# Kernel tuning notes

Measured on AMD Instinct MI355X. Metric: run time of the kernel, lower is better.

The kernel has to match this reference:

```python
import jax, jax.numpy as jnp
from jax import lax
import numpy as np

B = 8; T = 64000
NFFT = 1024; HOP = 256
SC = 20; KS = 1024; PAD = 512
HEADS = 8; GH = 64; GO = 32
SPEC_DIM = 32 * (NFFT // 4) // 2   # 4096
NODE_DIM = SC + SPEC_DIM           # 4116
EPS = 1e-5
NEG_SLOPE = 0.2


def setup_inputs() -> dict:
    ks = jax.random.split(jax.random.key(0), 12)
    f32 = jnp.float32
    def rn(k, shp, s):
        return jax.random.normal(k, shp, dtype=f32) * s
    return {
        "x": jax.random.normal(ks[0], (B, 1, T), dtype=f32),
        "sinc_w": rn(ks[1], (SC, 1, KS), 0.03),
        "conv1_w": rn(ks[2], (32, 1, 3, 3), 0.1),
        "conv1_b": jnp.zeros((32,), f32),
        "bn1_g": jnp.ones((32,), f32),
        "bn1_b": jnp.zeros((32,), f32),
        "conv2_w": rn(ks[3], (32, 32, 3, 3), 0.06),
        "conv2_b": jnp.zeros((32,), f32),
        "bn2_g": jnp.ones((32,), f32),
        "bn2_b": jnp.zeros((32,), f32),
        "gat1_W": rn(ks[4], (NODE_DIM, HEADS * GH), 0.015),
        "gat1_asrc": rn(ks[5], (HEADS, GH), 0.1),
        "gat1_adst": rn(ks[6], (HEADS, GH), 0.1),
        "gat1_bias": jnp.zeros((HEADS * GH,), f32),
        "gat2_W": rn(ks[7], (HEADS * GH, GO), 0.04),
        "gat2_asrc": rn(ks[8], (1, GO), 0.1),
        "gat2_adst": rn(ks[9], (1, GO), 0.1),
        "gat2_bias": jnp.zeros((GO,), f32),
        "fc1_w": rn(ks[10], (GO, 128), 0.15),
        "fc1_b": jnp.zeros((128,), f32),
        "bnf_g": jnp.ones((128,), f32),
        "bnf_b": jnp.zeros((128,), f32),
        "fc2_w": rn(ks[11], (128, 2), 0.08),
        "fc2_b": jnp.zeros((2,), f32),
    }


def _bn2d_eval(z, g, b):
    # eval-mode BatchNorm2d with running_mean=0, running_var=1
    s = g / jnp.sqrt(1.0 + EPS)
    return z * s[None, :, None, None] + b[None, :, None, None]


def _conv2d(z, w, b):
    y = lax.conv_general_dilated(z, w, (1, 1), ((1, 1), (1, 1)),
                                 dimension_numbers=("NCHW", "OIHW", "NCHW"))
    return y + b[None, :, None, None]


def _gat_dense(hin, W, asrc, adst, bias, heads, fo, concat):
    # PyG GATConv on a fully-connected graph (add_self_loops=True default
    # => every node attends to all nodes including itself). Eval mode (no dropout).
    b, n, d = hin.shape
    h = jnp.einsum("bnd,dhf->bnhf", hin, W.reshape(d, heads, fo))
    s_src = jnp.einsum("bnhf,hf->bnh", h, asrc)   # alpha_j contribution
    s_dst = jnp.einsum("bnhf,hf->bnh", h, adst)   # alpha_i contribution
    e = jax.nn.leaky_relu(s_dst[:, :, None, :] + s_src[:, None, :, :], NEG_SLOPE)  # (b,i,j,h)
    a = jax.nn.softmax(e, axis=2)                 # softmax over sources j per dest i
    out = jnp.einsum("bijh,bjhf->bihf", a, h)
    out = out.reshape(b, n, heads * fo) if concat else out.mean(axis=2)
    return out + bias


def reference(x, sinc_w, conv1_w, conv1_b, bn1_g, bn1_b, conv2_w, conv2_b,
              bn2_g, bn2_b, gat1_W, gat1_asrc, gat1_adst, gat1_bias,
              gat2_W, gat2_asrc, gat2_adst, gat2_bias,
              fc1_w, fc1_b, bnf_g, bnf_b, fc2_w, fc2_b):
    b = x.shape[0]
    # --- sinc (band-pass) conv branch: conv1d k=1024, pad=512 ---
    sinc = lax.conv_general_dilated(x, sinc_w, (1,), ((PAD, PAD),),
                                    dimension_numbers=("NCH", "OIH", "NCH"))  # (b,20,T+1)
    Ls = (sinc.shape[-1] // 4) * 4
    sinc_feat = sinc[:, :, :Ls].reshape(b, SC, Ls // 4, 4).mean(-1)  # avg_pool1d(4)
    sinc_feat = jnp.transpose(sinc_feat, (0, 2, 1))                  # (b, Ls//4, 20)

    # --- STFT branch (torch.stft: center=True, reflect pad, rect window) ---
    xw = x[:, 0, :]
    xp = jnp.pad(xw, ((0, 0), (NFFT // 2, NFFT // 2)), mode="reflect")
    n_frames = 1 + T // HOP  # 251
    idx = np.arange(n_frames)[:, None] * HOP + np.arange(NFFT)
    frames = xp[:, idx]                                   # (b, 251, 1024)
    mag = jnp.abs(jnp.fft.rfft(frames, axis=-1))          # (b, 251, 513)
    logmag = jnp.log(mag + 1e-9)
    s = jnp.transpose(logmag, (0, 2, 1))[:, None]         # (b, 1, 513, 251)

    h = jax.nn.relu(_bn2d_eval(_conv2d(s, conv1_w, conv1_b), bn1_g, bn1_b))
    h = jax.nn.relu(_bn2d_eval(_conv2d(h, conv2_w, conv2_b), bn2_g, bn2_b))
    Fq = (h.shape[2] // 2) * 2
    Tt = (h.shape[3] // 2) * 2
    h = h[:, :, :Fq, :Tt].reshape(b, 32, Fq // 2, 2, Tt // 2, 2).max(axis=(3, 5))  # maxpool 2x2
    spec_feat = jnp.transpose(h, (0, 3, 1, 2)).reshape(b, -1, SPEC_DIM)  # (b, 250, 4096)

    n = min(sinc_feat.shape[1], spec_feat.shape[1])  # 250
    nodes = jnp.concatenate([sinc_feat[:, :n], spec_feat[:, :n]], axis=-1)  # (b,250,4116)

    g1 = jax.nn.relu(_gat_dense(nodes, gat1_W, gat1_asrc, gat1_adst, gat1_bias, HEADS, GH, True))
    g2 = _gat_dense(g1, gat2_W, gat2_asrc, gat2_adst, gat2_bias, 1, GO, False)
    emb = g2.mean(axis=1)  # (b, 32) graph-mean readout

    z = emb @ fc1_w + fc1_b
    z = jax.nn.relu(z * (bnf_g / jnp.sqrt(1.0 + EPS)) + bnf_b)  # eval BN1d
    out = z @ fc2_w + fc2_b
    return (out, emb)
```

## Files before the change

kernel.cpp:

```cpp
#include <hip/hip_runtime.h>
#include <hip/hip_bf16.h>
#include <math.h>

#define TB 8
#define TT 64000
#define NFRAMES 251
#define NROWS (TB*NFRAMES)
#define GROWS 2048
#define NBINS 513
#define NBPAD 576
#define NNODE 250
#define NODE_DIM 4116
#define KPAD 4128

typedef __attribute__((ext_vector_type(8))) short short8;
typedef __attribute__((ext_vector_type(4))) float floatx4;

static __device__ __forceinline__ unsigned short f2bf(float x) {
    __hip_bfloat16 h = __float2bfloat16(x);
    return *(unsigned short*)&h;
}
static __device__ __forceinline__ float bf2f(unsigned short u) {
    __hip_bfloat16 h = *(__hip_bfloat16*)&u;
    return __bfloat162float(h);
}

__global__ __launch_bounds__(256) void k_prep(
    const float* __restrict__ x, const float* __restrict__ sinc_w,
    const float* __restrict__ c2w, const float* __restrict__ g2bn,
    const float* __restrict__ c1w, const float* __restrict__ g1bn,
    const float* __restrict__ W,
    unsigned short* __restrict__ fh, unsigned short* __restrict__ fl,
    unsigned short* __restrict__ bch, unsigned short* __restrict__ bcl,
    unsigned short* __restrict__ bsh, unsigned short* __restrict__ bsl,
    unsigned short* __restrict__ wbt, unsigned short* __restrict__ Bp,
    unsigned short* __restrict__ Bc1,
    unsigned short* __restrict__ Wt, unsigned short* __restrict__ nodesb,
    unsigned short* __restrict__ h1t, unsigned short* __restrict__ h2t) {
    __shared__ unsigned short tile[64][65];
    int bi = blockIdx.x, tid = threadIdx.x;
    if (bi < 2048) {
        int idx = bi * 256 + tid;
        int row = idx >> 8, r = idx & 255;
        int b = row >> 8, j = row & 255;
        int u = j * 256 + r - 512;
        if (u < 0) u = -u;
        if (u >= TT) u = 2 * TT - 2 - u;
        float v = x[b * TT + u];
        unsigned short h = f2bf(v);
        fh[idx] = h;
        fl[idx] = f2bf(v - bf2f(h));
    } else if (bi < 2624) {
        int idx = (bi - 2048) * 256 + tid;
        int k = idx >> 8, r = idx & 255;
        float s = 0.f, c = 0.f;
        if (k < NBINS) {
            int mm = (k * r) & 1023;
            sincospif((float)mm * (1.0f / 512.0f), &s, &c);
        }
        unsigned short chv = f2bf(c), shv = f2bf(s);
        bch[idx] = chv; bcl[idx] = f2bf(c - bf2f(chv));
        bsh[idx] = shv; bsl[idx] = f2bf(s - bf2f(shv));
    } else if (bi < 3144) {
        int local = bi - 2624;
        int kt = local % 65, nt = local / 65;
        for (int idx = tid; idx < 4096; idx += 256) {
            int r = idx >> 6, c = idx & 63;
            int kp = kt * 64 + r;
            int k;
            if (kp < 20) k = kp;
            else if (kp < NODE_DIM) { int t = kp - 20; k = 20 + (t & 15) * 256 + (t >> 4); }
            else k = -1;
            float v = (k >= 0) ? W[k * 512 + nt * 64 + c] : 0.f;
            tile[r][c] = f2bf(v);
        }
        __syncthreads();
        for (int idx = tid; idx < 4096; idx += 256) {
            int nl = idx >> 6, kl = idx & 63;
            int k = kt * 64 + kl;
            if (k < KPAD)
                Wt[(size_t)(nt * 64 + nl) * KPAD + k] = tile[kl][nl];
        }
    } else if (bi < 3276) {
        int idx = (bi - 3144) * 256 + tid;
        if (idx < 32 * 1056) {
            int c = idx / 1056, m = idx - c * 1056;
            float s = 0.f;
            if (c < 20 && m < 1027) {
                #pragma unroll
                for (int d = 0; d < 4; d++) {
                    int k = m - d;
                    if (k >= 0 && k < 1024) s += sinc_w[c * 1024 + k];
                }
                s *= 0.25f;
            }
            wbt[idx] = f2bf(s);
        }
    } else if (bi < 3312) {
        int idx = (bi - 3276) * 256 + tid;
        if (idx < 9216) {
            int j = idx & 7, lane = (idx >> 3) & 63, ct = (idx >> 9) & 1, s = idx >> 10;
            int co = ct * 16 + (lane & 15);
            int ci = (lane >> 4) * 8 + j;
            float inv = rsqrtf(1.0f + 1e-5f);
            Bp[idx] = f2bf(c2w[co * 288 + ci * 9 + s] * (g2bn[co] * inv));
        }
    } else if (bi < 3508) {
        int idx = (bi - 3312) * 256 + tid;
        if (idx < 24000) {
            int row = idx / 12, c = idx - row * 12;
            nodesb[(size_t)row * KPAD + 4116 + c] = 0;
        } else if (idx < 48576) {
            int t = idx - 24000; int r = t / 6, c = t - r * 6;
            h1t[(size_t)r * 256 + 250 + c] = 0;
        } else if (idx < 50112) {
            int t = idx - 48576; int r = t / 6, c = t - r * 6;
            h2t[(size_t)r * 256 + 250 + c] = 0;
        }
    } else {
        int idx = (bi - 3508) * 256 + tid;
        if (idx < 1024) {
            int ch = idx >> 5, k = idx & 31;
            float inv = rsqrtf(1.0f + 1e-5f);
            int t; int typ;
            if (k < 8)       { t = k;      typ = 0; }
            else if (k < 16) { t = k - 8;  typ = 0; }
            else if (k < 24) { t = k - 16; typ = 1; }
            else if (k == 24 || k == 25) { t = 8; typ = 0; }
            else if (k == 26) { t = 8; typ = 1; }
            else { t = 0; typ = 2; }
            unsigned short outv = 0;
            if (typ != 2) {
                float wv = c1w[ch * 9 + t] * (g1bn[ch] * inv);
                unsigned short whi = f2bf(wv);
                outv = (typ == 0) ? whi : f2bf(wv - bf2f(whi));
            }
            Bc1[idx] = outv;
        }
    }
}

__global__ __launch_bounds__(256) void k_sincm(const float* __restrict__ x,
                                               const unsigned short* __restrict__ wbt,
                                               unsigned short* __restrict__ nodesb) {
    __shared__ __align__(16) unsigned short xs[1312];
    int ut = blockIdx.x, b = blockIdx.y;
    int tid = threadIdx.x;
    int base = 256 * ut - 512;
    for (int i = tid; i < 1312; i += 256) {
        int g = base + i;
        float v = (g >= 0 && g < TT) ? x[b * TT + g] : 0.f;
        xs[i] = f2bf(v);
    }
    __syncthreads();
    int w = tid >> 6, lane = tid & 63;
    int q = lane >> 4, col = lane & 15;
    floatx4 acc[2];
    acc[0] = acc[1] = (floatx4){0.f, 0.f, 0.f, 0.f};
    for (int K0 = 0; K0 < 1056; K0 += 32) {
        int off = 4 * (w * 16 + col) + K0 + q * 8;
        unsigned long long lo = *(const unsigned long long*)&xs[off];
        unsigned long long hi = *(const unsigned long long*)&xs[off + 4];
        union { unsigned long long u64[2]; short8 s8; } cv;
        cv.u64[0] = lo; cv.u64[1] = hi;
        short8 af = cv.s8;
        #pragma unroll
        for (int ni = 0; ni < 2; ni++) {
            short8 bf = *(const short8*)(wbt + (size_t)(ni * 16 + col) * 1056 + K0 + q * 8);
            acc[ni] = __builtin_amdgcn_mfma_f32_16x16x32_bf16(af, bf, acc[ni], 0, 0, 0);
        }
    }
    #pragma unroll
    for (int ni = 0; ni < 2; ni++)
        #pragma unroll
        for (int rr = 0; rr < 4; rr++) {
            int u = ut * 64 + w * 16 + q * 4 + rr;
            int c = ni * 16 + col;
            if (u < NNODE && c < 20)
                nodesb[(size_t)(b * NNODE + u) * KPAD + c] = f2bf(acc[ni][rr]);
        }
}

__global__ __launch_bounds__(256) void k_dft_mfma(const unsigned short* __restrict__ fh,
                                                  const unsigned short* __restrict__ fl,
                                                  const unsigned short* __restrict__ ch,
                                                  const unsigned short* __restrict__ cl,
                                                  const unsigned short* __restrict__ sh,
                                                  const unsigned short* __restrict__ sl,
                                                  float* __restrict__ GRo,
                                                  float* __restrict__ GIo) {
    __shared__ __align__(16) unsigned short Ah[32 * 40];
    __shared__ __align__(16) unsigned short Al[32 * 40];
    __shared__ __align__(16) unsigned short Bch[64 * 40];
    __shared__ __align__(16) unsigned short Bcl[64 * 40];
    __shared__ __align__(16) unsigned short Bsh[64 * 40];
    __shared__ __align__(16) unsigned short Bsl[64 * 40];
    int tid = threadIdx.x;
    int N0 = blockIdx.x * 64, M0 = blockIdx.y * 32;
    int br = tid >> 2, bc = (tid & 3) * 8;
    size_t boff = (size_t)(N0 + br) * 256 + bc;
    int ar = (tid & 127) >> 2, ac = (tid & 3) * 8;
    size_t aoff = (size_t)(M0 + ar) * 256 + ac;
    bool loA = tid < 128;
    int w = tid >> 6, lane = tid & 63;
    int q = lane >> 4, col = lane & 15;
    int mb = (w >> 1) * 16, nb = (w & 1) * 32;
    floatx4 aR[2], aI[2];
    aR[0] = aR[1] = aI[0] = aI[1] = (floatx4){0.f, 0.f, 0.f, 0.f};

    for (int K0 = 0; K0 < 256; K0 += 32) {
        if (loA) *(short8*)&Ah[ar * 40 + ac] = *(const short8*)(fh + aoff + K0);
        else     *(short8*)&Al[ar * 40 + ac] = *(const short8*)(fl + aoff + K0);
        *(short8*)&Bch[br * 40 + bc] = *(const short8*)(ch + boff + K0);
        *(short8*)&Bcl[br * 40 + bc] = *(const short8*)(cl + boff + K0);
        *(short8*)&Bsh[br * 40 + bc] = *(const short8*)(sh + boff + K0);
        *(short8*)&Bsl[br * 40 + bc] = *(const short8*)(sl + boff + K0);
        __syncthreads();
        short8 ahv = *(const short8*)&Ah[(mb + col) * 40 + q * 8];
        short8 alv = *(const short8*)&Al[(mb + col) * 40 + q * 8];
        #pragma unroll
        for (int ni = 0; ni < 2; ni++) {
            short8 chv = *(const short8*)&Bch[(nb + ni * 16 + col) * 40 + q * 8];
            short8 clv = *(const short8*)&Bcl[(nb + ni * 16 + col) * 40 + q * 8];
            short8 shv = *(const short8*)&Bsh[(nb + ni * 16 + col) * 40 + q * 8];
            short8 slv = *(const short8*)&Bsl[(nb + ni * 16 + col) * 40 + q * 8];
            aR[ni] = __builtin_amdgcn_mfma_f32_16x16x32_bf16(ahv, chv, aR[ni], 0, 0, 0);
            aR[ni] = __builtin_amdgcn_mfma_f32_16x16x32_bf16(ahv, clv, aR[ni], 0, 0, 0);
            aR[ni] = __builtin_amdgcn_mfma_f32_16x16x32_bf16(alv, chv, aR[ni], 0, 0, 0);
            aI[ni] = __builtin_amdgcn_mfma_f32_16x16x32_bf16(ahv, shv, aI[ni], 0, 0, 0);
            aI[ni] = __builtin_amdgcn_mfma_f32_16x16x32_bf16(ahv, slv, aI[ni], 0, 0, 0);
            aI[ni] = __builtin_amdgcn_mfma_f32_16x16x32_bf16(alv, shv, aI[ni], 0, 0, 0);
        }
        __syncthreads();
    }
    #pragma unroll
    for (int ni = 0; ni < 2; ni++)
        #pragma unroll
        for (int rr = 0; rr < 4; rr++) {
            int m = M0 + mb + q * 4 + rr;
            int bin = N0 + nb + ni * 16 + col;
            GRo[(size_t)m * NBPAD + bin] = aR[ni][rr];
            GIo[(size_t)m * NBPAD + bin] = aI[ni][rr];
        }
}

__global__ __launch_bounds__(256) void k_dftcomb(const float* __restrict__ GR,
                                                 const float* __restrict__ GI,
                                                 float* __restrict__ S0) {
    int idx = blockIdx.x * 256 + threadIdx.x;
    if (idx >= NROWS * NBINS) return;
    int mg = idx / NBINS, bin = idx - mg * NBINS;
    int b = mg / NFRAMES, i = mg - b * NFRAMES;
    size_t base = ((size_t)(b * 256 + i)) * NBPAD + bin;
    float gr0 = GR[base], gr1 = GR[base + NBPAD], gr2 = GR[base + 2 * NBPAD], gr3 = GR[base + 3 * NBPAD];
    float gs0 = GI[base], gs1 = GI[base + NBPAD], gs2 = GI[base + 2 * NBPAD], gs3 = GI[base + 3 * NBPAD];
    float fre, fim;
    switch (bin & 3) {
        case 0: fre = gr0 + gr1 + gr2 + gr3; fim = gs0 + gs1 + gs2 + gs3; break;
        case 1: fre = gr0 - gs1 - gr2 + gs3; fim = gs0 + gr1 - gs2 - gr3; break;
        case 2: fre = gr0 - gr1 + gr2 - gr3; fim = gs0 - gs1 + gs2 - gs3; break;
        default: fre = gr0 + gs1 - gr2 - gs3; fim = gs0 - gr1 - gs2 + gr3; break;
    }
    S0[(b * NBINS + bin) * NFRAMES + i] = logf(sqrtf(fmaf(fre, fre, fim * fim)) + 1e-9f);
}

#define O1STR 40
__global__ __launch_bounds__(256) void k_conv2f(const float* __restrict__ S0,
                                                const unsigned short* __restrict__ Bc1,
                                                const float* __restrict__ c1b,
                                                const float* __restrict__ g1bn,
                                                const float* __restrict__ b1bn,
                                                const unsigned short* __restrict__ Bp,
                                                const float* __restrict__ c2b,
                                                const float* __restrict__ g2bn,
                                                const float* __restrict__ b2bn,
                                                unsigned short* __restrict__ nodesb) {
    __shared__ __align__(16) unsigned short o1s[18 * 18 * O1STR];
    __shared__ float S0s[20][20];
    __shared__ float b1s[32];
    __shared__ float b2s[32];
    int tid = threadIdx.x;
    int b = blockIdx.z;
    int F0 = blockIdx.y * 8;
    int T0 = blockIdx.x * 8;
    float inv = rsqrtf(1.0f + 1e-5f);
    if (tid < 32) {
        b1s[tid] = c1b[tid] * (g1bn[tid] * inv) + b1bn[tid];
        b2s[tid] = c2b[tid] * (g2bn[tid] * inv) + b2bn[tid];
    }
    for (int i = tid; i < 400; i += 256) {
        int r = i / 20, c = i - r * 20;
        int rr = 2 * F0 - 2 + r, cc = 2 * T0 - 2 + c;
        float v = 0.f;
        if (rr >= 0 && rr < 513 && cc >= 0 && cc < 251)
            v = S0[((size_t)b * 513 + rr) * 251 + cc];
        S0s[r][c] = v;
    }
    __syncthreads();

    int lane = tid & 63, w = tid >> 6;
    int q = lane >> 4, col = lane & 15;

    {
        short8 bfr0 = *(const short8*)(Bc1 + (size_t)col * 32 + q * 8);
        short8 bfr1 = *(const short8*)(Bc1 + (size_t)(16 + col) * 32 + q * 8);
        for (int mt = w; mt < 21; mt += 4) {
            int p = mt * 16 + col;
            int pc = p < 324 ? p : 0;
            int pr = (pc * 228) >> 12;
            int pt = pc - pr * 18;
            float tv[9];
            #pragma unroll
            for (int di = 0; di < 3; di++)
                #pragma unroll
                for (int dj = 0; dj < 3; dj++)
                    tv[di * 3 + dj] = S0s[pr + di][pt + dj];
            unsigned short hu[9], lu[9];
            #pragma unroll
            for (int i = 0; i < 9; i++) {
                hu[i] = f2bf(tv[i]);
                lu[i] = f2bf(tv[i] - bf2f(hu[i]));
            }
            short8 af;
            if (q == 1) {
                af[0] = lu[0]; af[1] = lu[1]; af[2] = lu[2]; af[3] = lu[3];
                af[4] = lu[4]; af[5] = lu[5]; af[6] = lu[6]; af[7] = lu[7];
            } else if (q == 3) {
                af[0] = hu[8]; af[1] = lu[8]; af[2] = hu[8]; af[3] = 0;
                af[4] = 0; af[5] = 0; af[6] = 0; af[7] = 0;
            } else {
                af[0] = hu[0]; af[1] = hu[1]; af[2] = hu[2]; af[3] = hu[3];
                af[4] = hu[4]; af[5] = hu[5]; af[6] = hu[6]; af[7] = hu[7];
            }
            floatx4 c0 = (floatx4){0.f, 0.f, 0.f, 0.f};
            floatx4 c1 = (floatx4){0.f, 0.f, 0.f, 0.f};
            c0 = __builtin_amdgcn_mfma_f32_16x16x32_bf16(af, bfr0, c0, 0, 0, 0);
            c1 = __builtin_amdgcn_mfma_f32_16x16x32_bf16(af, bfr1, c1, 0, 0, 0);
            #pragma unroll
            for (int rr2 = 0; rr2 < 4; rr2++) {
                int pp = mt * 16 + q * 4 + rr2;
                if (pp < 324) {
                    int qr = (pp * 228) >> 12, qt = pp - qr * 18;
                    int r1 = 2 * F0 - 1 + qr, t1 = 2 * T0 - 1 + qt;
                    bool valid = (r1 >= 0 && r1 < 513 && t1 >= 0 && t1 < 251);
                    float v0 = fmaxf(c0[rr2] + b1s[col], 0.f);
                    float v1 = fmaxf(c1[rr2] + b1s[16 + col], 0.f);
                    o1s[pp * O1STR + col]      = valid ? f2bf(v0) : (unsigned short)0;
                    o1s[pp * O1STR + 16 + col] = valid ? f2bf(v1) : (unsigned short)0;
                }
            }
        }
    }
    __syncthreads();

    floatx4 acc[4][2];
    #pragma unroll
    for (int rt = 0; rt < 4; rt++)
        #pragma unroll
        for (int ct = 0; ct < 2; ct++)
            acc[rt][ct] = (floatx4){0.f, 0.f, 0.f, 0.f};

    #pragma unroll
    for (int s = 0; s < 9; s++) {
        const int di = s / 3, dj = s % 3;
        short8 bf0 = *(const short8*)&Bp[(s * 2 + 0) * 512 + lane * 8];
        short8 bf1 = *(const short8*)&Bp[(s * 2 + 1) * 512 + lane * 8];
        #pragma unroll
        for (int rt = 0; rt < 4; rt++) {
            short8 af = *(const short8*)&o1s[((w * 4 + rt + di) * 18 + (col + dj)) * O1STR + q * 8];
            acc[rt][0] = __builtin_amdgcn_mfma_f32_16x16x32_bf16(af, bf0, acc[rt][0], 0, 0, 0);
            acc[rt][1] = __builtin_amdgcn_mfma_f32_16x16x32_bf16(af, bf1, acc[rt][1], 0, 0, 0);
        }
    }
    __syncthreads();

    unsigned short* nb = o1s;
    #pragma unroll
    for (int ct = 0; ct < 2; ct++) {
        float bb = b2s[ct * 16 + col];
        #pragma unroll
        for (int fp2 = 0; fp2 < 2; fp2++)
            #pragma unroll
            for (int tc2 = 0; tc2 < 2; tc2++) {
                float m0 = fmaxf(
                    fmaxf(acc[2 * fp2][ct][2 * tc2], acc[2 * fp2][ct][2 * tc2 + 1]),
                    fmaxf(acc[2 * fp2 + 1][ct][2 * tc2], acc[2 * fp2 + 1][ct][2 * tc2 + 1]));
                float v = fmaxf(m0 + bb, 0.f);
                int nl = (2 * q + tc2) * 2 + ct;
                int fl = 2 * w + fp2;
                nb[nl * 136 + fl * 16 + col] = f2bf(v);
            }
    }
    __syncthreads();

    int nl = tid >> 4, part = tid & 15;
    int node_g = 2 * T0 + nl;
    if (node_g < NNODE) {
        unsigned short* dst = nodesb + (size_t)(b * NNODE + node_g) * KPAD + 20 + F0 * 16 + part * 8;
        *(short8*)(dst) = *(const short8*)&nb[nl * 136 + part * 8];
    }
}

__global__ __launch_bounds__(256) void k_gat1s(const unsigned short* __restrict__ A,
                                               const unsigned short* __restrict__ Bt,
                                               float* __restrict__ hpart) {
    __shared__ __align__(16) unsigned short As[64 * 40];
    __shared__ __align__(16) unsigned short Bs[64 * 40];
    int tid = threadIdx.x;
    int N0 = blockIdx.x * 64, M0 = blockIdx.y * 64;
    int kc = blockIdx.z;
    int ks = (kc == 0) ? 0 : (33 + 32 * (kc - 1));
    int ke = 33 + 32 * kc;
    if (kc == 0) ke = 33;
    int sr = tid >> 2, sc = (tid & 3) * 8;
    int w = tid >> 6, lane = tid & 63;
    int q = lane >> 4, col = lane & 15;
    int mb = (w >> 1) * 32, nb = (w & 1) * 32;
    floatx4 acc[2][2];
    acc[0][0] = acc[0][1] = acc[1][0] = acc[1][1] = (floatx4){0.f, 0.f, 0.f, 0.f};
    short8 z8 = {0, 0, 0, 0, 0, 0, 0, 0};
    int mA = M0 + sr;
    bool mv = mA < 2000;
    const unsigned short* pa = A + (size_t)mA * KPAD + sc;
    const unsigned short* pb = Bt + (size_t)(N0 + sr) * KPAD + sc;

    for (int kk = ks; kk < ke; kk++) {
        int K0 = kk * 32;
        short8 va = mv ? *(const short8*)(pa + K0) : z8;
        short8 vb = *(const short8*)(pb + K0);
        *(short8*)&As[sr * 40 + sc] = va;
        *(short8*)&Bs[sr * 40 + sc] = vb;
        __syncthreads();
        short8 a0 = *(const short8*)&As[(mb + col) * 40 + q * 8];
        short8 a1 = *(const short8*)&As[(mb + 16 + col) * 40 + q * 8];
        short8 b0 = *(const short8*)&Bs[(nb + col) * 40 + q * 8];
        short8 b1 = *(const short8*)&Bs[(nb + 16 + col) * 40 + q * 8];
        acc[0][0] = __builtin_amdgcn_mfma_f32_16x16x32_bf16(a0, b0, acc[0][0], 0, 0, 0);
        acc[0][1] = __builtin_amdgcn_mfma_f32_16x16x32_bf16(a0, b1, acc[0][1], 0, 0, 0);
        acc[1][0] = __builtin_amdgcn_mfma_f32_16x16x32_bf16(a1, b0, acc[1][0], 0, 0, 0);
        acc[1][1] = __builtin_amdgcn_mfma_f32_16x16x32_bf16(a1, b1, acc[1][1], 0, 0, 0);
        __syncthreads();
    }
    float* out = hpart + (size_t)kc * 1024000;
    #pragma unroll
    for (int mi = 0; mi < 2; mi++)
        #pragma unroll
        for (int ni = 0; ni < 2; ni++)
            #pragma unroll
            for (int rr = 0; rr < 4; rr++) {
                int m = M0 + mb + mi * 16 + q * 4 + rr;
                if (m < 2000)
                    out[m * 512 + N0 + nb + ni * 16 + col] = acc[mi][ni][rr];
            }
}

__global__ __launch_bounds__(256) void k_hred(const float* __restrict__ hpart,
                                              const float* __restrict__ asrc,
                                              const float* __restrict__ adst,
                                              unsigned short* __restrict__ h1t,
                                              float* __restrict__ ssrc,
                                              float* __restrict__ sdst) {
    int m = blockIdx.x;
    int tid = threadIdx.x;
    int n1 = tid, n2 = tid + 256;
    size_t base = (size_t)m * 512;
    float s1 = hpart[base + n1] + hpart[base + n1 + 1024000] +
               hpart[base + n1 + 2048000] + hpart[base + n1 + 3072000];
    float s2 = hpart[base + n2] + hpart[base + n2 + 1024000] +
               hpart[base + n2 + 2048000] + hpart[base + n2 + 3072000];
    int bb = m / NNODE, j = m - bb * NNODE;
    int hh1 = n1 >> 6, f1 = n1 & 63;
    int hh2 = n2 >> 6, f2 = n2 & 63;
    h1t[((size_t)((bb * 8 + hh1) * 64 + f1)) * 256 + j] = f2bf(s1);
    h1t[((size_t)((bb * 8 + hh2) * 64 + f2)) * 256 + j] = f2bf(s2);
    float ps1 = s1 * asrc[n1], pd1 = s1 * adst[n1];
    float ps2 = s2 * asrc[n2], pd2 = s2 * adst[n2];
    for (int off = 32; off > 0; off >>= 1) {
        ps1 += __shfl_down(ps1, off); pd1 += __shfl_down(pd1, off);
        ps2 += __shfl_down(ps2, off); pd2 += __shfl_down(pd2, off);
    }
    int lane = tid & 63, w = tid >> 6;
    if (lane == 0) {
        ssrc[m * 8 + w] = ps1;     sdst[m * 8 + w] = pd1;
        ssrc[m * 8 + 4 + w] = ps2; sdst[m * 8 + 4 + w] = pd2;
    }
}

#define PSTR 264
__global__ __launch_bounds__(256) void k_att1(const float* __restrict__ ssrc,
                                              const float* __restrict__ sdst,
                                              const unsigned short* __restrict__ h1t,
                                              const float* __restrict__ bias,
                                              float* __restrict__ g1) {
    __shared__ __align__(16) unsigned short Ps[128 * PSTR];
    __shared__ float ss[NNODE];
    __shared__ float red[4];
    int mhalf = blockIdx.x, bh = blockIdx.y;
    int b = bh >> 3, h = bh & 7;
    int tid = threadIdx.x;
    for (int j = tid; j < NNODE; j += 256) ss[j] = ssrc[(b * NNODE + j) * 8 + h];
    __syncthreads();
    float mv = (tid < NNODE) ? ss[tid] : -1e30f;
    for (int off = 32; off > 0; off >>= 1) mv = fmaxf(mv, __shfl_down(mv, off));
    if ((tid & 63) == 0) red[tid >> 6] = mv;
    __syncthreads();
    float smaxv = fmaxf(fmaxf(red[0], red[1]), fmaxf(red[2], red[3]));
    if (tid < 128) {
        unsigned short* row = Ps + tid * PSTR;
        int row_g = mhalf * 128 + tid;
        short8 z8 = {0, 0, 0, 0, 0, 0, 0, 0};
        if (row_g >= NNODE) {
            #pragma unroll
            for (int j = 0; j < 256; j += 8) *(short8*)(row + j) = z8;
        } else {
            float d = sdst[(b * NNODE + row_g) * 8 + h];
            float e0 = d + smaxv;
            float mx = e0 > 0.f ? e0 : 0.2f * e0;
            float den = 0.f;
            for (int j = 0; j < NNODE; j++) {
                float e = d + ss[j];
                e = e > 0.f ? e : 0.2f * e;
                den += __expf(e - mx);
            }
            float rden = 1.f / den;
            for (int j0 = 0; j0 < 256; j0 += 8) {
                unsigned short wv[8];
                #pragma unroll
                for (int jj = 0; jj < 8; jj++) {
                    int j = j0 + jj;
                    float wt = 0.f;
                    if (j < NNODE) {
                        float e = d + ss[j];
                        e = e > 0.f ? e : 0.2f * e;
                        wt = __expf(e - mx) * rden;
                    }
                    wv[jj] = f2bf(wt);
                }
                *(short8*)(row + j0) = *(const short8*)wv;
            }
        }
    }
    __syncthreads();
    int w = tid >> 6, lane = tid & 63;
    int q = lane >> 4, col = lane & 15;
    const unsigned short* Hb = h1t + (size_t)bh * 16384;
    floatx4 acc[2][4];
    #pragma unroll
    for (int mi = 0; mi < 2; mi++)
        #pragma unroll
        for (int ni = 0; ni < 4; ni++)
            acc[mi][ni] = (floatx4){0.f, 0.f, 0.f, 0.f};
    for (int k0 = 0; k0 < 256; k0 += 32) {
        short8 af[2], bf[4];
        #pragma unroll
        for (int mi = 0; mi < 2; mi++)
            af[mi] = *(const short8*)&Ps[((w * 2 + mi) * 16 + col) * PSTR + k0 + q * 8];
        #pragma unroll
        for (int ni = 0; ni < 4; ni++)
            bf[ni] = *(const short8*)(Hb + (size_t)(ni * 16 + col) * 256 + k0 + q * 8);
        #pragma unroll
        for (int mi = 0; mi < 2; mi++)
            #pragma unroll
            for (int ni = 0; ni < 4; ni++)
                acc[mi][ni] = __builtin_amdgcn_mfma_f32_16x16x32_bf16(af[mi], bf[ni], acc[mi][ni], 0, 0, 0);
    }
    #pragma unroll
    for (int mi = 0; mi < 2; mi++)
        #pragma unroll
        for (int ni = 0; ni < 4; ni++)
            #pragma unroll
            for (int rr = 0; rr < 4; rr++) {
                int i = mhalf * 128 + (w * 2 + mi) * 16 + q * 4 + rr;
                int f = ni * 16 + col;
                if (i < NNODE)
                    g1[(b * NNODE + i) * 512 + h * 64 + f] =
                        fmaxf(acc[mi][ni][rr] + bias[h * 64 + f], 0.f);
            }
}

__global__ __launch_bounds__(256) void k_h2(const float* __restrict__ g1,
                                            const float* __restrict__ W2,
                                            const float* __restrict__ a2src,
                                            const float* __restrict__ a2dst,
                                            unsigned short* __restrict__ h2t,
                                            float* __restrict__ s2src,
                                            float* __restrict__ s2dst) {
    int row = blockIdx.x * 4 + (threadIdx.x >> 6);
    if (row >= 2000) return;
    int lane = threadIdx.x & 63;
    int o = lane & 31, half = lane >> 5;
    const float* gr = &g1[row * 512 + half * 256];
    float acc = 0.f;
    for (int k = 0; k < 256; k++) acc = fmaf(gr[k], W2[(half * 256 + k) * 32 + o], acc);
    acc += __shfl_down(acc, 32);
    float ps = acc * a2src[o], pd = acc * a2dst[o];
    for (int off = 16; off > 0; off >>= 1) {
        ps += __shfl_down(ps, off, 32);
        pd += __shfl_down(pd, off, 32);
    }
    if (lane == 0) { s2src[row] = ps; s2dst[row] = pd; }
    if (lane < 32) {
        int b = row / NNODE, j = row - b * NNODE;
        h2t[((size_t)(b * 32 + o)) * 256 + j] = f2bf(acc);
    }
}

__global__ __launch_bounds__(256) void k_att2(const float* __restrict__ s2src,
                                              const float* __restrict__ s2dst,
                                              const unsigned short* __restrict__ h2t,
                                              const float* __restrict__ bias2,
                                              float* __restrict__ g2) {
    __shared__ __align__(16) unsigned short Ps[256 * PSTR];
    __shared__ float ss[NNODE];
    __shared__ float red[4];
    int b = blockIdx.x;
    int tid = threadIdx.x;
    for (int j = tid; j < NNODE; j += 256) ss[j] = s2src[b * NNODE + j];
    __syncthreads();
    float mv = (tid < NNODE) ? ss[tid] : -1e30f;
    for (int off = 32; off > 0; off >>= 1) mv = fmaxf(mv, __shfl_down(mv, off));
    if ((tid & 63) == 0) red[tid >> 6] = mv;
    __syncthreads();
    float smaxv = fmaxf(fmaxf(red[0], red[1]), fmaxf(red[2], red[3]));
    {
        unsigned short* row = Ps + tid * PSTR;
        short8 z8 = {0, 0, 0, 0, 0, 0, 0, 0};
        if (tid >= NNODE) {
            #pragma unroll
            for (int j = 0; j < 256; j += 8) *(short8*)(row + j) = z8;
        } else {
            float d = s2dst[b * NNODE + tid];
            float e0 = d + smaxv;
            float mx = e0 > 0.f ? e0 : 0.2f * e0;
            float den = 0.f;
            for (int j = 0; j < NNODE; j++) {
                float e = d + ss[j];
                e = e > 0.f ? e : 0.2f * e;
                den += __expf(e - mx);
            }
            float rden = 1.f / den;
            for (int j0 = 0; j0 < 256; j0 += 8) {
                unsigned short wv[8];
                #pragma unroll
                for (int jj = 0; jj < 8; jj++) {
                    int j = j0 + jj;
                    float wt = 0.f;
                    if (j < NNODE) {
                        float e = d + ss[j];
                        e = e > 0.f ? e : 0.2f * e;
                        wt = __expf(e - mx) * rden;
                    }
                    wv[jj] = f2bf(wt);
                }
                *(short8*)(row + j0) = *(const short8*)wv;
            }
        }
    }
    __syncthreads();
    int w = tid >> 6, lane = tid & 63;
    int q = lane >> 4, col = lane & 15;
    const unsigned short* Hb = h2t + (size_t)b * 8192;
    floatx4 acc[4][2];
    #pragma unroll
    for (int mi = 0; mi < 4; mi++)
        #pragma unroll
        for (int ni = 0; ni < 2; ni++)
            acc[mi][ni] = (floatx4){0.f, 0.f, 0.f, 0.f};
    for (int k0 = 0; k0 < 256; k0 += 32) {
        short8 af[4], bf[2];
        #pragma unroll
        for (int mi = 0; mi < 4; mi++)
            af[mi] = *(const short8*)&Ps[((w * 4 + mi) * 16 + col) * PSTR + k0 + q * 8];
        #pragma unroll
        for (int ni = 0; ni < 2; ni++)
            bf[ni] = *(const short8*)(Hb + (size_t)(ni * 16 + col) * 256 + k0 + q * 8);
        #pragma unroll
        for (int mi = 0; mi < 4; mi++)
            #pragma unroll
            for (int ni = 0; ni < 2; ni++)
                acc[mi][ni] = __builtin_amdgcn_mfma_f32_16x16x32_bf16(af[mi], bf[ni], acc[mi][ni], 0, 0, 0);
    }
    #pragma unroll
    for (int mi = 0; mi < 4; mi++)
        #pragma unroll
        for (int ni = 0; ni < 2; ni++)
            #pragma unroll
            for (int rr = 0; rr < 4; rr++) {
                int i = (w * 4 + mi) * 16 + q * 4 + rr;
                int f = ni * 16 + col;
                if (i < NNODE)
                    g2[(b * NNODE + i) * 32 + f] = acc[mi][ni][rr] + bias2[f];
            }
}

__global__ __launch_bounds__(256) void k_fc(const float* __restrict__ g2,
                                            const float* __restrict__ fc1w,
                                            const float* __restrict__ fc1b,
                                            const float* __restrict__ bnfg,
                                            const float* __restrict__ bnfb,
                                            const float* __restrict__ fc2w,
                                            const float* __restrict__ fc2b,
                                            float* __restrict__ dout) {
    __shared__ float es[256];
    __shared__ float zs[1024];
    int tid = threadIdx.x;
    {
        int b = tid >> 5, f = tid & 31;
        float s = 0.f;
        #pragma unroll 5
        for (int i = 0; i < NNODE; i++) s += g2[((size_t)(b * NNODE + i)) * 32 + f];
        s *= (1.0f / 250.0f);
        es[tid] = s;
        dout[16 + tid] = s;
    }
    __syncthreads();
    float inv = rsqrtf(1.0f + 1e-5f);
    #pragma unroll
    for (int rep = 0; rep < 4; rep++) {
        int idx = tid + rep * 256;
        int b = idx >> 7, j = idx & 127;
        float a = fc1b[j];
        #pragma unroll
        for (int k = 0; k < 32; k++) a = fmaf(es[b * 32 + k], fc1w[k * 128 + j], a);
        a = a * (bnfg[j] * inv) + bnfb[j];
        zs[idx] = fmaxf(a, 0.f);
    }
    __syncthreads();
    if (tid < 16) {
        int b = tid >> 1, o = tid & 1;
        float a = fc2b[o];
        for (int k = 0; k < 128; k++) a = fmaf(zs[b * 128 + k], fc2w[k * 2 + o], a);
        dout[b * 2 + o] = a;
    }
}

extern "C" void kernel_launch(void* const* d_in, const int* in_sizes, int n_in,
                              void* d_out, int out_size, void* d_ws, size_t ws_size,
                              hipStream_t stream) {
    (void)in_sizes; (void)n_in; (void)out_size; (void)ws_size;
    const float* x       = (const float*)d_in[0];
    const float* sinc_w  = (const float*)d_in[1];
    const float* conv1_w = (const float*)d_in[2];
    const float* conv1_b = (const float*)d_in[3];
    const float* bn1_g   = (const float*)d_in[4];
    const float* bn1_b   = (const float*)d_in[5];
    const float* conv2_w = (const float*)d_in[6];
    const float* conv2_b = (const float*)d_in[7];
    const float* bn2_g   = (const float*)d_in[8];
    const float* bn2_b   = (const float*)d_in[9];
    const float* gat1_W  = (const float*)d_in[10];
    const float* gat1_as = (const float*)d_in[11];
    const float* gat1_ad = (const float*)d_in[12];
    const float* gat1_bi = (const float*)d_in[13];
    const float* gat2_W  = (const float*)d_in[14];
    const float* gat2_as = (const float*)d_in[15];
    const float* gat2_ad = (const float*)d_in[16];
    const float* gat2_bi = (const float*)d_in[17];
    const float* fc1_w   = (const float*)d_in[18];
    const float* fc1_b   = (const float*)d_in[19];
    const float* bnf_g   = (const float*)d_in[20];
    const float* bnf_b   = (const float*)d_in[21];
    const float* fc2_w   = (const float*)d_in[22];
    const float* fc2_b   = (const float*)d_in[23];
    float* dout = (float*)d_out;

    unsigned short* fh  = (unsigned short*)d_ws;
    unsigned short* fl  = fh + (size_t)GROWS * 256;
    unsigned short* bch = fl + (size_t)GROWS * 256;
    unsigned short* bcl = bch + (size_t)NBPAD * 256;
    unsigned short* bsh = bcl + (size_t)NBPAD * 256;
    unsigned short* bsl = bsh + (size_t)NBPAD * 256;
    float* GRb = (float*)(bsl + (size_t)NBPAD * 256);
    float* GIb = GRb + (size_t)GROWS * NBPAD;
    float* S0  = GIb + (size_t)GROWS * NBPAD;
    unsigned short* wbt = (unsigned short*)(S0 + 1030104);
    unsigned short* bpk = wbt + 32 * 1056;
    unsigned short* Bc1 = bpk + 9216;
    unsigned short* Wt  = Bc1 + 1024;
    unsigned short* nodesb = Wt + (size_t)512 * KPAD;
    unsigned short* Pn  = nodesb + (size_t)2000 * KPAD;
    unsigned short* h1t = Pn + (size_t)64 * 256 * 256;
    unsigned short* h2t = h1t + (size_t)64 * 64 * 256;
    unsigned short* P2n = h2t + (size_t)8 * 32 * 256;
    float* hpart = (float*)(P2n + (size_t)8 * 256 * 256);
    float* ssrc1 = hpart + 4 * 1024000;
    float* sdst1 = ssrc1 + 16000;
    float* g1    = sdst1 + 16000;
    float* s2src = g1 + 1024000;
    float* s2dst = s2src + 2000;
    float* g2    = s2dst + 2000;

    hipLaunchKernelGGL(k_prep, dim3(3512), dim3(256), 0, stream,
                       x, sinc_w, conv2_w, bn2_g, conv1_w, bn1_g, gat1_W,
                       fh, fl, bch, bcl, bsh, bsl, wbt, bpk, Bc1, Wt, nodesb, h1t, h2t);
    hipLaunchKernelGGL(k_dft_mfma, dim3(9, 64), dim3(256), 0, stream,
                       fh, fl, bch, bcl, bsh, bsl, GRb, GIb);
    hipLaunchKernelGGL(k_dftcomb, dim3((NROWS * NBINS + 255) / 256), dim3(256), 0, stream,
                       GRb, GIb, S0);
    hipLaunchKernelGGL(k_sincm, dim3(4, 8), dim3(256), 0, stream, x, wbt, nodesb);
    hipLaunchKernelGGL(k_conv2f, dim3(16, 32, 8), dim3(256), 0, stream,
                       S0, Bc1, conv1_b, bn1_g, bn1_b, bpk, conv2_b, bn2_g, bn2_b, nodesb);
    hipLaunchKernelGGL(k_gat1s, dim3(8, 32, 4), dim3(256), 0, stream, nodesb, Wt, hpart);
    hipLaunchKernelGGL(k_hred, dim3(2000), dim3(256), 0, stream,
                       hpart, gat1_as, gat1_ad, h1t, ssrc1, sdst1);
    hipLaunchKernelGGL(k_att1, dim3(2, 64), dim3(256), 0, stream,
                       ssrc1, sdst1, h1t, gat1_bi, g1);
    hipLaunchKernelGGL(k_h2, dim3(500), dim3(256), 0, stream,
                       g1, gat2_W, gat2_as, gat2_ad, h2t, s2src, s2dst);
    hipLaunchKernelGGL(k_att2, dim3(8), dim3(256), 0, stream,
                       s2src, s2dst, h2t, gat2_bi, g2);
    hipLaunchKernelGGL(k_fc, dim3(1), dim3(256), 0, stream,
                       g2, fc1_w, fc1_b, bnf_g, bnf_b, fc2_w, fc2_b, dout);
}
```

Before: 327.5 us.

## Merge sinc conv into DFT kernel and fuse DFT combine into conv2f load

Packs the sinc-filter MFMA blocks and the DFT GEMM blocks into a single launch, with the sinc work on the trailing block indices. The DFT results are now written transposed (bin-major, frame-contiguous) through an LDS staging tile. The separate dftcomb kernel is removed: conv2f applies the radix-4 combine, magnitude and log directly as it loads its input tile, so the S0 intermediate is never written or read. This cuts two launches and one full-size round trip through global memory. In exchange, conv2f recomputes the combine for halo elements shared by neighbouring tiles, and the DFT epilogue gains extra LDS passes and barriers.

```diff
diff --git a/kernel.cpp b/kernel.cpp
--- a/kernel.cpp
+++ b/kernel.cpp
@@ -140,63 +140,67 @@
     }
 }
 
-__global__ __launch_bounds__(256) void k_sincm(const float* __restrict__ x,
-                                               const unsigned short* __restrict__ wbt,
-                                               unsigned short* __restrict__ nodesb) {
-    __shared__ __align__(16) unsigned short xs[1312];
-    int ut = blockIdx.x, b = blockIdx.y;
+__global__ __launch_bounds__(256) void k_dftsinc(const unsigned short* __restrict__ fh,
+                                                 const unsigned short* __restrict__ fl,
+                                                 const unsigned short* __restrict__ ch,
+                                                 const unsigned short* __restrict__ cl,
+                                                 const unsigned short* __restrict__ sh,
+                                                 const unsigned short* __restrict__ sl,
+                                                 float* __restrict__ GTR,
+                                                 float* __restrict__ GTI,
+                                                 const float* __restrict__ x,
+                                                 const unsigned short* __restrict__ wbt,
+                                                 unsigned short* __restrict__ nodesb) {
+    __shared__ __align__(16) unsigned char smem[34048];
     int tid = threadIdx.x;
-    int base = 256 * ut - 512;
-    for (int i = tid; i < 1312; i += 256) {
-        int g = base + i;
-        float v = (g >= 0 && g < TT) ? x[b * TT + g] : 0.f;
-        xs[i] = f2bf(v);
-    }
-    __syncthreads();
-    int w = tid >> 6, lane = tid & 63;
-    int q = lane >> 4, col = lane & 15;
-    floatx4 acc[2];
-    acc[0] = acc[1] = (floatx4){0.f, 0.f, 0.f, 0.f};
-    for (int K0 = 0; K0 < 1056; K0 += 32) {
-        int off = 4 * (w * 16 + col) + K0 + q * 8;
-        unsigned long long lo = *(const unsigned long long*)&xs[off];
-        unsigned long long hi = *(const unsigned long long*)&xs[off + 4];
-        union { unsigned long long u64[2]; short8 s8; } cv;
-        cv.u64[0] = lo; cv.u64[1] = hi;
-        short8 af = cv.s8;
-        #pragma unroll
-        for (int ni = 0; ni < 2; ni++) {
-            short8 bf = *(const short8*)(wbt + (size_t)(ni * 16 + col) * 1056 + K0 + q * 8);
-            acc[ni] = __builtin_amdgcn_mfma_f32_16x16x32_bf16(af, bf, acc[ni], 0, 0, 0);
-        }
-    }
-    #pragma unroll
-    for (int ni = 0; ni < 2; ni++)
-        #pragma unroll
-        for (int rr = 0; rr < 4; rr++) {
-            int u = ut * 64 + w * 16 + q * 4 + rr;
-            int c = ni * 16 + col;
-            if (u < NNODE && c < 20)
-                nodesb[(size_t)(b * NNODE + u) * KPAD + c] = f2bf(acc[ni][rr]);
-        }
-}
-
-__global__ __launch_bounds__(256) void k_dft_mfma(const unsigned short* __restrict__ fh,
-                                                  const unsigned short* __restrict__ fl,
-                                                  const unsigned short* __restrict__ ch,
-                                                  const unsigned short* __restrict__ cl,
-                                                  const unsigned short* __restrict__ sh,
-                                                  const unsigned short* __restrict__ sl,
-                                                  float* __restrict__ GRo,
-                                                  float* __restrict__ GIo) {
-    __shared__ __align__(16) unsigned short Ah[32 * 40];
-    __shared__ __align__(16) unsigned short Al[32 * 40];
-    __shared__ __align__(16) unsigned short Bch[64 * 40];
-    __shared__ __align__(16) unsigned short Bcl[64 * 40];
-    __shared__ __align__(16) unsigned short Bsh[64 * 40];
-    __shared__ __align__(16) unsigned short Bsl[64 * 40];
-    int tid = threadIdx.x;
-    int N0 = blockIdx.x * 64, M0 = blockIdx.y * 32;
+    int bi = blockIdx.x;
+    if (bi >= 576) {
+        unsigned short* xs = (unsigned short*)smem;
+        int local = bi - 576;
+        int ut = local & 3, b = local >> 2;
+        int base = 256 * ut - 512;
+        for (int i = tid; i < 1312; i += 256) {
+            int g = base + i;
+            float v = (g >= 0 && g < TT) ? x[b * TT + g] : 0.f;
+            xs[i] = f2bf(v);
+        }
+        __syncthreads();
+        int w = tid >> 6, lane = tid & 63;
+        int q = lane >> 4, col = lane & 15;
+        floatx4 acc[2];
+        acc[0] = acc[1] = (floatx4){0.f, 0.f, 0.f, 0.f};
+        for (int K0 = 0; K0 < 1056; K0 += 32) {
+            int off = 4 * (w * 16 + col) + K0 + q * 8;
+            unsigned long long lo = *(const unsigned long long*)&xs[off];
+            unsigned long long hi = *(const unsigned long long*)&xs[off + 4];
+            union { unsigned long long u64[2]; short8 s8; } cv;
+            cv.u64[0] = lo; cv.u64[1] = hi;
+            short8 af = cv.s8;
+            #pragma unroll
+            for (int ni = 0; ni < 2; ni++) {
+                short8 bf = *(const short8*)(wbt + (size_t)(ni * 16 + col) * 1056 + K0 + q * 8);
+                acc[ni] = __builtin_amdgcn_mfma_f32_16x16x32_bf16(af, bf, acc[ni], 0, 0, 0);
+            }
+        }
+        #pragma unroll
+        for (int ni = 0; ni < 2; ni++)
+            #pragma unroll
+            for (int rr = 0; rr < 4; rr++) {
+                int u = ut * 64 + w * 16 + q * 4 + rr;
+                int c = ni * 16 + col;
+                if (u < NNODE && c < 20)
+                    nodesb[(size_t)(b * NNODE + u) * KPAD + c] = f2bf(acc[ni][rr]);
+            }
+        return;
+    }
+    unsigned short* Ah  = (unsigned short*)smem;
+    unsigned short* Al  = (unsigned short*)(smem + 2560);
+    unsigned short* Bch = (unsigned short*)(smem + 5120);
+    unsigned short* Bcl = (unsigned short*)(smem + 10240);
+    unsigned short* Bsh = (unsigned short*)(smem + 15360);
+    unsigned short* Bsl = (unsigned short*)(smem + 20480);
+    float* TR = (float*)(smem + 25600);
+    int N0 = (bi % 9) * 64, M0 = (bi / 9) * 32;
     int br = tid >> 2, bc = (tid & 3) * 8;
     size_t boff = (size_t)(N0 + br) * 256 + bc;
     int ar = (tid & 127) >> 2, ac = (tid & 3) * 8;
@@ -233,39 +237,35 @@
         }
         __syncthreads();
     }
+    int bin_l = tid >> 2, ms = (tid & 3) * 8;
     #pragma unroll
     for (int ni = 0; ni < 2; ni++)
         #pragma unroll
-        for (int rr = 0; rr < 4; rr++) {
-            int m = M0 + mb + q * 4 + rr;
-            int bin = N0 + nb + ni * 16 + col;
-            GRo[(size_t)m * NBPAD + bin] = aR[ni][rr];
-            GIo[(size_t)m * NBPAD + bin] = aI[ni][rr];
-        }
-}
-
-__global__ __launch_bounds__(256) void k_dftcomb(const float* __restrict__ GR,
-                                                 const float* __restrict__ GI,
-                                                 float* __restrict__ S0) {
-    int idx = blockIdx.x * 256 + threadIdx.x;
-    if (idx >= NROWS * NBINS) return;
-    int mg = idx / NBINS, bin = idx - mg * NBINS;
-    int b = mg / NFRAMES, i = mg - b * NFRAMES;
-    size_t base = ((size_t)(b * 256 + i)) * NBPAD + bin;
-    float gr0 = GR[base], gr1 = GR[base + NBPAD], gr2 = GR[base + 2 * NBPAD], gr3 = GR[base + 3 * NBPAD];
-    float gs0 = GI[base], gs1 = GI[base + NBPAD], gs2 = GI[base + 2 * NBPAD], gs3 = GI[base + 3 * NBPAD];
-    float fre, fim;
-    switch (bin & 3) {
-        case 0: fre = gr0 + gr1 + gr2 + gr3; fim = gs0 + gs1 + gs2 + gs3; break;
-        case 1: fre = gr0 - gs1 - gr2 + gs3; fim = gs0 + gr1 - gs2 - gr3; break;
-        case 2: fre = gr0 - gr1 + gr2 - gr3; fim = gs0 - gs1 + gs2 - gs3; break;
-        default: fre = gr0 + gs1 - gr2 - gs3; fim = gs0 - gr1 - gs2 + gr3; break;
-    }
-    S0[(b * NBINS + bin) * NFRAMES + i] = logf(sqrtf(fmaf(fre, fre, fim * fim)) + 1e-9f);
+        for (int rr = 0; rr < 4; rr++)
+            TR[(nb + ni * 16 + col) * 33 + mb + q * 4 + rr] = aR[ni][rr];
+    __syncthreads();
+    {
+        float* dst = GTR + (size_t)(N0 + bin_l) * 2048 + M0 + ms;
+        #pragma unroll
+        for (int j = 0; j < 8; j++) dst[j] = TR[bin_l * 33 + ms + j];
+    }
+    __syncthreads();
+    #pragma unroll
+    for (int ni = 0; ni < 2; ni++)
+        #pragma unroll
+        for (int rr = 0; rr < 4; rr++)
+            TR[(nb + ni * 16 + col) * 33 + mb + q * 4 + rr] = aI[ni][rr];
+    __syncthreads();
+    {
+        float* dst = GTI + (size_t)(N0 + bin_l) * 2048 + M0 + ms;
+        #pragma unroll
+        for (int j = 0; j < 8; j++) dst[j] = TR[bin_l * 33 + ms + j];
+    }
 }
 
 #define O1STR 40
-__global__ __launch_bounds__(256) void k_conv2f(const float* __restrict__ S0,
+__global__ __launch_bounds__(256) void k_conv2f(const float* __restrict__ GTR,
+                                                const float* __restrict__ GTI,
                                                 const unsigned short* __restrict__ Bc1,
                                                 const float* __restrict__ c1b,
                                                 const float* __restrict__ g1bn,
@@ -290,10 +290,21 @@
     }
     for (int i = tid; i < 400; i += 256) {
         int r = i / 20, c = i - r * 20;
-        int rr = 2 * F0 - 2 + r, cc = 2 * T0 - 2 + c;
+        int bin = 2 * F0 - 2 + r, fr = 2 * T0 - 2 + c;
         float v = 0.f;
-        if (rr >= 0 && rr < 513 && cc >= 0 && cc < 251)
-            v = S0[((size_t)b * 513 + rr) * 251 + cc];
+        if (bin >= 0 && bin < 513 && fr >= 0 && fr < 251) {
+            size_t base = (size_t)bin * 2048 + b * 256 + fr;
+            float gr0 = GTR[base], gr1 = GTR[base + 1], gr2 = GTR[base + 2], gr3 = GTR[base + 3];
+            float gs0 = GTI[base], gs1 = GTI[base + 1], gs2 = GTI[base + 2], gs3 = GTI[base + 3];
+            float fre, fim;
+            switch (bin & 3) {
+                case 0: fre = gr0 + gr1 + gr2 + gr3; fim = gs0 + gs1 + gs2 + gs3; break;
+                case 1: fre = gr0 - gs1 - gr2 + gs3; fim = gs0 + gr1 - gs2 - gr3; break;
+                case 2: fre = gr0 - gr1 + gr2 - gr3; fim = gs0 - gs1 + gs2 - gs3; break;
+                default: fre = gr0 + gs1 - gr2 - gs3; fim = gs0 - gr1 - gs2 + gr3; break;
+            }
+            v = logf(sqrtf(fmaf(fre, fre, fim * fim)) + 1e-9f);
+        }
         S0s[r][c] = v;
     }
     __syncthreads();
@@ -770,9 +781,9 @@
     unsigned short* bcl = bch + (size_t)NBPAD * 256;
     unsigned short* bsh = bcl + (size_t)NBPAD * 256;
     unsigned short* bsl = bsh + (size_t)NBPAD * 256;
-    float* GRb = (float*)(bsl + (size_t)NBPAD * 256);
-    float* GIb = GRb + (size_t)GROWS * NBPAD;
-    float* S0  = GIb + (size_t)GROWS * NBPAD;
+    float* GTR = (float*)(bsl + (size_t)NBPAD * 256);
+    float* GTI = GTR + (size_t)GROWS * NBPAD;
+    float* S0  = GTI + (size_t)GROWS * NBPAD;
     unsigned short* wbt = (unsigned short*)(S0 + 1030104);
     unsigned short* bpk = wbt + 32 * 1056;
     unsigned short* Bc1 = bpk + 9216;
@@ -793,13 +804,10 @@
     hipLaunchKernelGGL(k_prep, dim3(3512), dim3(256), 0, stream,
                        x, sinc_w, conv2_w, bn2_g, conv1_w, bn1_g, gat1_W,
                        fh, fl, bch, bcl, bsh, bsl, wbt, bpk, Bc1, Wt, nodesb, h1t, h2t);
-    hipLaunchKernelGGL(k_dft_mfma, dim3(9, 64), dim3(256), 0, stream,
-                       fh, fl, bch, bcl, bsh, bsl, GRb, GIb);
-    hipLaunchKernelGGL(k_dftcomb, dim3((NROWS * NBINS + 255) / 256), dim3(256), 0, stream,
-                       GRb, GIb, S0);
-    hipLaunchKernelGGL(k_sincm, dim3(4, 8), dim3(256), 0, stream, x, wbt, nodesb);
+    hipLaunchKernelGGL(k_dftsinc, dim3(608), dim3(256), 0, stream,
+                       fh, fl, bch, bcl, bsh, bsl, GTR, GTI, x, wbt, nodesb);
     hipLaunchKernelGGL(k_conv2f, dim3(16, 32, 8), dim3(256), 0, stream,
-                       S0, Bc1, conv1_b, bn1_g, bn1_b, bpk, conv2_b, bn2_g, bn2_b, nodesb);
+                       GTR, GTI, Bc1, conv1_b, bn1_g, bn1_b, bpk, conv2_b, bn2_g, bn2_b, nodesb);
     hipLaunchKernelGGL(k_gat1s, dim3(8, 32, 4), dim3(256), 0, stream, nodesb, Wt, hpart);
     hipLaunchKernelGGL(k_hred, dim3(2000), dim3(256), 0, stream,
                        hpart, gat1_as, gat1_ad, h1t, ssrc1, sdst1);
```

After: 313.2 us. 1.05x faster.
